# Optimization experiments

Measured on AMD Instinct MI355X. Metric: run time of the kernel, lower is better.

The kernel has to match this reference:

```python
import jax, jax.numpy as jnp
import numpy as np

B = 1024          # batch
H = 512           # hidden_dim
T = 256           # seq_len
CD = 2            # coord_dim
LAT = 64 + 64 + 128  # total latent dim


def setup_inputs() -> dict:
    key = jax.random.key(0)
    ks = jax.random.split(key, 20)
    s = 0.05  # weight init scale
    rn = lambda k, shp: (jax.random.normal(k, shp, dtype=jnp.float32) * s)
    return {
        "z_primitive": jax.random.normal(ks[0], (B, 64), dtype=jnp.float32),
        "z_skill": jax.random.normal(ks[1], (B, 64), dtype=jnp.float32),
        "z_style": jax.random.normal(ks[2], (B, 128), dtype=jnp.float32),
        "W_proj": rn(ks[3], (2 * H, LAT)),
        "b_proj": jnp.zeros((2 * H,), jnp.float32),
        "Wih1": rn(ks[4], (4 * H, CD)),
        "Whh1": rn(ks[5], (4 * H, H)),
        "bih1": jnp.zeros((4 * H,), jnp.float32),
        "bhh1": jnp.zeros((4 * H,), jnp.float32),
        "Wih2": rn(ks[6], (4 * H, H)),
        "Whh2": rn(ks[7], (4 * H, H)),
        "bih2": jnp.zeros((4 * H,), jnp.float32),
        "bhh2": jnp.zeros((4 * H,), jnp.float32),
        "Wo1": rn(ks[8], (H // 2, H)),
        "bo1": jnp.zeros((H // 2,), jnp.float32),
        "Wo2": rn(ks[9], (CD, H // 2)),
        "bo2": jnp.zeros((CD,), jnp.float32),
    }


def _lstm_cell(x, h, c, Wih, Whh, bih, bhh):
    # PyTorch gate order: i, f, g, o
    gates = x @ Wih.T + h @ Whh.T + (bih + bhh)
    i, f, g, o = jnp.split(gates, 4, axis=1)
    c_new = jax.nn.sigmoid(f) * c + jax.nn.sigmoid(i) * jnp.tanh(g)
    h_new = jax.nn.sigmoid(o) * jnp.tanh(c_new)
    return h_new, c_new


def reference(z_primitive, z_skill, z_style, W_proj, b_proj,
              Wih1, Whh1, bih1, bhh1, Wih2, Whh2, bih2, bhh2,
              Wo1, bo1, Wo2, bo2):
    z = jnp.concatenate([z_primitive, z_skill, z_style], axis=1)  # [B, LAT]
    init = z @ W_proj.T + b_proj                                  # [B, 2H]
    h0 = init[:, :H]
    c0 = init[:, H:]
    x0 = jnp.zeros((z.shape[0], CD), init.dtype)

    def step(carry, _):
        x, h1, c1, h2, c2 = carry
        h1, c1 = _lstm_cell(x, h1, c1, Wih1, Whh1, bih1, bhh1)
        h2, c2 = _lstm_cell(h1, h2, c2, Wih2, Whh2, bih2, bhh2)
        # output MLP (Dropout inactive in eval)
        y = jax.nn.relu(h2 @ Wo1.T + bo1) @ Wo2.T + bo2  # [B, CD]
        return (y, h1, c1, h2, c2), y

    # h0/c0 repeated across both LSTM layers (repeat(2,1,1) in torch)
    _, ys = jax.lax.scan(step, (x0, h0, c0, h0, c0), None, length=T)
    return jnp.transpose(ys, (1, 0, 2))  # [B, T, CD]
```

## Files before the change

kernel.cpp:

```cpp
#include <hip/hip_runtime.h>
#include <math.h>

#define NB 1024
#define NH 512
#define NT 256
#define NCD 2

typedef unsigned short u16;
typedef __bf16 bf16x8 __attribute__((ext_vector_type(8)));
typedef float  f32x4  __attribute__((ext_vector_type(4)));

#define MFMA_BF16 __builtin_amdgcn_mfma_f32_16x16x32_bf16

__device__ __forceinline__ float sigf(float x) { return 1.0f / (1.0f + expf(-x)); }
__device__ __forceinline__ u16 f2b(float f) {
    union { float f; unsigned i; } v; v.f = f;
    unsigned r = v.i + 0x7fffu + ((v.i >> 16) & 1u);
    return (u16)(r >> 16);
}

__device__ __forceinline__ void async_cp16(const void* gptr, void* lptr) {
    __builtin_amdgcn_global_load_lds(
        (const __attribute__((address_space(1))) unsigned int*)gptr,
        (__attribute__((address_space(3))) unsigned int*)lptr,
        16, 0, 0);
}

__device__ __forceinline__ float aloadf(const float* p) {
    return __hip_atomic_load((float*)p, __ATOMIC_RELAXED, __HIP_MEMORY_SCOPE_AGENT);
}

__global__ __launch_bounds__(256) void convert3(
    const float* __restrict__ a, const float* __restrict__ b,
    const float* __restrict__ c,
    u16* __restrict__ oa, u16* __restrict__ ob, u16* __restrict__ oc)
{
    const int i = blockIdx.x * 256 + threadIdx.x;
    oa[i] = f2b(a[i]); ob[i] = f2b(b[i]); oc[i] = f2b(c[i]);
}

__global__ __launch_bounds__(256) void convw1(
    const float* __restrict__ a, u16* __restrict__ o)
{
    const int i = blockIdx.x * 256 + threadIdx.x;
    o[i] = f2b(a[i]);
}

__global__ __launch_bounds__(256) void bsum_k(
    const float* __restrict__ bi1, const float* __restrict__ bh1,
    const float* __restrict__ bi2, const float* __restrict__ bh2,
    float* __restrict__ o1, float* __restrict__ o2)
{
    const int i = blockIdx.x * 256 + threadIdx.x;
    o1[i] = bi1[i] + bh1[i];
    o2[i] = bi2[i] + bh2[i];
}

__global__ __launch_bounds__(512) void zero_bar(unsigned* __restrict__ b)
{
    b[threadIdx.x] = 0u;
}

__global__ __launch_bounds__(512) void zero_out(float* __restrict__ o)
{
    o[blockIdx.x * 512 + threadIdx.x] = 0.f;
}

__global__ __launch_bounds__(256) void init_kernel(
    const float* __restrict__ zp, const float* __restrict__ zs,
    const float* __restrict__ zst, const float* __restrict__ Wp,
    const float* __restrict__ bp,
    u16* __restrict__ h1, float* __restrict__ c1,
    u16* __restrict__ h2, float* __restrict__ c2)
{
    __shared__ float z[4][256];
    const int tid = threadIdx.x;
    const int b0  = blockIdx.x * 4;
    for (int i = tid; i < 4 * 256; i += 256) {
        const int bb = i >> 8, k = i & 255;
        float v;
        if (k < 64)       v = zp [(b0 + bb) * 64  + k];
        else if (k < 128) v = zs [(b0 + bb) * 64  + (k - 64)];
        else              v = zst[(b0 + bb) * 128 + (k - 128)];
        z[bb][k] = v;
    }
    __syncthreads();
    for (int rt = 0; rt < 4; ++rt) {
        const int r = rt * 256 + tid;
        const float bias = bp[r];
        float a0 = bias, a1 = bias, a2 = bias, a3 = bias;
        for (int k = 0; k < 256; ++k) {
            const float w = Wp[r * 256 + k];
            a0 += z[0][k] * w; a1 += z[1][k] * w;
            a2 += z[2][k] * w; a3 += z[3][k] * w;
        }
        const float acc[4] = {a0, a1, a2, a3};
        for (int bb = 0; bb < 4; ++bb) {
            const int b = b0 + bb;
            if (r < NH) {
                h1[b * NH + r] = f2b(acc[bb]);
                h2[b * NH + r] = f2b(acc[bb]);
            } else {
                c1[b * NH + r - NH] = acc[bb];
                c2[b * NH + r - NH] = acc[bb];
            }
        }
    }
}

__global__ __launch_bounds__(512, 4) void fused_out_lstm1(
    const u16* __restrict__ h2prev,
    const u16* __restrict__ A0,
    const u16* __restrict__ W0,
    const float* __restrict__ bsum,
    const float* __restrict__ Wx,
    const u16* __restrict__ W1b,
    const float* __restrict__ bo1, const float* __restrict__ Wo2,
    const float* __restrict__ bo2, float* __restrict__ outp,
    float* __restrict__ c, u16* __restrict__ hnext,
    unsigned* __restrict__ bar,
    const int t, const int do_lstm)
{
    __shared__ __align__(16) char smem[61440];
    float* eg  = (float*)smem;

    const int tid  = threadIdx.x;
    const int lane = tid & 63;
    const int wv   = tid >> 6;
    const int g    = wv & 3;
    const int mh   = wv >> 2;
    const int l15  = lane & 15;
    const int q    = lane >> 4;
    const int bx   = blockIdx.x;
    const int ut   = (bx & 7) * 2 + ((bx >> 3) & 1);
    const int grp  = bx >> 4;
    const int b0   = grp * 32;
    const int u0   = ut * 32;

    int goffW0, goffW1, goffA = 0, goffWS = 0;
    {
        const int c0 = (wv * 2) * 64 + lane;
        const int w0r = c0 >> 3;
        goffW0 = ((w0r >> 5) * NH + u0 + (w0r & 31)) * NH + (((c0 & 7) ^ (w0r & 7)) * 8);
        const int c1i = (wv * 2 + 1) * 64 + lane;
        const int w1r = c1i >> 3;
        goffW1 = ((w1r >> 5) * NH + u0 + (w1r & 31)) * NH + (((c1i & 7) ^ (w1r & 7)) * 8);
        if (wv < 4) {
            const int ca = wv * 64 + lane;
            const int ar = ca >> 3;
            goffA = (b0 + ar) * NH + (((ca & 7) ^ (ar & 7)) * 8);
        }
        if (wv == 4 || wv == 5) {
            const int cs = (wv - 4) * 64 + lane;
            const int rl = cs >> 3;
            goffWS = (ut * 16 + rl) * NH + (((cs & 7) ^ (rl & 7)) * 8);
        }
    }

    auto issue = [&](int m, int bi) {
        const int k0 = (m & 7) * 64;
        char* base = smem + bi * 20480;
        async_cp16((const void*)(W0 + goffW0 + k0),
                   (void*)(base + 4096 + (wv * 2) * 1024));
        async_cp16((const void*)(W0 + goffW1 + k0),
                   (void*)(base + 4096 + (wv * 2 + 1) * 1024));
        if (wv < 4)
            async_cp16((const void*)(A0 + goffA + k0),
                       (void*)(base + wv * 1024));
    };

    const int u_e  = tid & 31;
    const int bq_e = tid >> 5;
    const int ug_e = u0 + u_e;
    float bs[4], wx0[4], wx1[4], cpre[2];
#pragma unroll
    for (int g4 = 0; g4 < 4; ++g4) bs[g4] = bsum[g4 * NH + ug_e];
#pragma unroll
    for (int g4 = 0; g4 < 4; ++g4) {
        wx0[g4] = Wx[(g4 * NH + ug_e) * 2 + 0];
        wx1[g4] = Wx[(g4 * NH + ug_e) * 2 + 1];
    }
    cpre[0] = c[(size_t)(b0 + bq_e * 2 + 0) * NH + ug_e];
    cpre[1] = c[(size_t)(b0 + bq_e * 2 + 1) * NH + ug_e];

    if (do_lstm) issue(0, 2);

    if (h2prev) {
        f32x4 acc_o[2];
        acc_o[0] = (f32x4){0.f, 0.f, 0.f, 0.f};
        acc_o[1] = (f32x4){0.f, 0.f, 0.f, 0.f};

        auto issue_pa = [&](int k, int pb) {
            const int k0 = k * 64;
            char* base = smem + pb * 8192;
            if (wv < 4)
                async_cp16((const void*)(h2prev + goffA + k0),
                           (void*)(base + (wv << 10)));
            if (wv == 4 || wv == 5)
                async_cp16((const void*)(W1b + goffWS + k0),
                           (void*)(base + 4096 + ((wv - 4) << 10)));
        };
        issue_pa(0, 0);
        issue_pa(1, 1);
        int cp = 0;
        for (int kk = 0; kk < 8; ++kk) {
            if (kk + 1 < 8)
                asm volatile("s_waitcnt vmcnt(1)" ::: "memory");
            else
                asm volatile("s_waitcnt vmcnt(0)" ::: "memory");
            __builtin_amdgcn_s_barrier();
            if (kk + 2 < 8) {
                int pb = cp + 2; if (pb >= 3) pb -= 3;
                issue_pa(kk + 2, pb);
            }
            const char* pbase = smem + cp * 8192;
#pragma unroll
            for (int kh = 0; kh < 2; ++kh) {
                const int j = (kh * 4 + q) ^ (l15 & 7);
                const bf16x8 bfr = *(const bf16x8*)(pbase + 4096 + l15 * 128 + j * 16);
#pragma unroll
                for (int mi = 0; mi < 2; ++mi) {
                    const bf16x8 av = *(const bf16x8*)(pbase + (mi * 16 + l15) * 128 + j * 16);
                    acc_o[mi] = MFMA_BF16(av, bfr, acc_o[mi], 0, 0, 0);
                }
            }
            ++cp; if (cp == 3) cp = 0;
        }
        const int ng = ut * 16 + l15;
        const float bo1n = bo1[ng];
        const float w20  = Wo2[ng];
        const float w21  = Wo2[256 + ng];
        float pa[2][4], pb[2][4];
#pragma unroll
        for (int mi = 0; mi < 2; ++mi)
#pragma unroll
            for (int r = 0; r < 4; ++r) {
                const float s = fmaxf(acc_o[mi][r] + bo1n, 0.f);
                pa[mi][r] = s * w20;
                pb[mi][r] = s * w21;
            }
#pragma unroll
        for (int off = 1; off < 16; off <<= 1)
#pragma unroll
            for (int mi = 0; mi < 2; ++mi)
#pragma unroll
                for (int r = 0; r < 4; ++r) {
                    pa[mi][r] += __shfl_xor(pa[mi][r], off, 64);
                    pb[mi][r] += __shfl_xor(pb[mi][r], off, 64);
                }
        if (wv == 0 && l15 == 0) {
            const float b20 = (ut == 0) ? bo2[0] : 0.f;
            const float b21 = (ut == 0) ? bo2[1] : 0.f;
#pragma unroll
            for (int mi = 0; mi < 2; ++mi)
#pragma unroll
                for (int r = 0; r < 4; ++r) {
                    const int m = mi * 16 + q * 4 + r;
                    float* dst = outp + (size_t)(b0 + m) * (NT * NCD) + (t - 1) * NCD;
                    atomicAdd(dst + 0, pa[mi][r] + b20);
                    atomicAdd(dst + 1, pb[mi][r] + b21);
                }
        }
        __syncthreads();
    }
    if (!do_lstm) return;

    f32x4 acc[2];
    acc[0] = (f32x4){0.f, 0.f, 0.f, 0.f};
    acc[1] = (f32x4){0.f, 0.f, 0.f, 0.f};
    const int M = 8;
    issue(1, 0);
    int ci = 2;
    for (int m = 0; m < M; ++m) {
        if (m + 1 < M) {
            if (wv < 4) asm volatile("s_waitcnt vmcnt(3)" ::: "memory");
            else        asm volatile("s_waitcnt vmcnt(2)" ::: "memory");
        } else {
            asm volatile("s_waitcnt vmcnt(0)" ::: "memory");
        }
        __builtin_amdgcn_s_barrier();
        if (m + 2 < M) {
            int bi = ci + 2; if (bi >= 3) bi -= 3;
            issue(m + 2, bi);
        }
        const char* bA = smem + ci * 20480;
        const char* bW = bA + 4096;
#pragma unroll
        for (int khi = 0; khi < 2; ++khi) {
            bf16x8 bfr[2];
#pragma unroll
            for (int ni = 0; ni < 2; ++ni) {
                const int wrow = g * 32 + ni * 16 + l15;
                const int j = (khi * 4 + q) ^ (wrow & 7);
                bfr[ni] = *(const bf16x8*)(bW + wrow * 128 + j * 16);
            }
            const int row = mh * 16 + l15;
            const int j = (khi * 4 + q) ^ (row & 7);
            const bf16x8 av = *(const bf16x8*)(bA + row * 128 + j * 16);
            acc[0] = MFMA_BF16(av, bfr[0], acc[0], 0, 0, 0);
            acc[1] = MFMA_BF16(av, bfr[1], acc[1], 0, 0, 0);
        }
        ++ci; if (ci == 3) ci = 0;
    }

    float r_x[4] = {0.f, 0.f, 0.f, 0.f};
    if (h2prev) {
        unsigned* mybar = bar + grp * 16;
        const unsigned target = 16u * (unsigned)t;
        __syncthreads();
        if (tid == 0) {
            __hip_atomic_fetch_add(mybar, 1u, __ATOMIC_RELAXED, __HIP_MEMORY_SCOPE_AGENT);
            int guard = 0;
            while (__hip_atomic_load(mybar, __ATOMIC_RELAXED, __HIP_MEMORY_SCOPE_AGENT)
                       < target && ++guard < (1 << 20)) {
                __builtin_amdgcn_s_sleep(1);
            }
        }
        __syncthreads();
#pragma unroll
        for (int jj = 0; jj < 2; ++jj) {
            const float* src = outp + (size_t)(b0 + bq_e * 2 + jj) * (NT * NCD)
                               + (t - 1) * NCD;
            r_x[jj * 2 + 0] = aloadf(src + 0);
            r_x[jj * 2 + 1] = aloadf(src + 1);
        }
    }

    __syncthreads();
#pragma unroll
    for (int ni = 0; ni < 2; ++ni)
#pragma unroll
        for (int r = 0; r < 4; ++r)
            eg[(g * 32 + mh * 16 + q * 4 + r) * 33 + ni * 16 + l15] = acc[ni][r];
    __syncthreads();

#pragma unroll
    for (int jj = 0; jj < 2; ++jj) {
        const int bl = bq_e * 2 + jj;
        const int b  = b0 + bl;
        float gv[4];
#pragma unroll
        for (int g4 = 0; g4 < 4; ++g4) gv[g4] = eg[(g4 * 32 + bl) * 33 + u_e] + bs[g4];
        const float x0 = r_x[jj * 2 + 0];
        const float x1 = r_x[jj * 2 + 1];
#pragma unroll
        for (int g4 = 0; g4 < 4; ++g4) gv[g4] += x0 * wx0[g4] + x1 * wx1[g4];
        const float iv = sigf(gv[0]);
        const float fv = sigf(gv[1]);
        const float gg = tanhf(gv[2]);
        const float ov = sigf(gv[3]);
        const size_t idx = (size_t)b * NH + ug_e;
        const float cn = fv * cpre[jj] + iv * gg;
        c[idx] = cn;
        hnext[idx] = f2b(ov * tanhf(cn));
    }
}

__global__ __launch_bounds__(512, 4) void lstm_mfma32(
    const u16* __restrict__ A0, const u16* __restrict__ W0,
    const u16* __restrict__ A1, const u16* __restrict__ W1,
    const float* __restrict__ bsum,
    float* __restrict__ c, u16* __restrict__ hnext,
    const int npass)
{
    __shared__ __align__(16) char smem[61440];
    float* eg = (float*)smem;

    const int tid  = threadIdx.x;
    const int lane = tid & 63;
    const int wv   = tid >> 6;
    const int g    = wv & 3;
    const int mh   = wv >> 2;
    const int l15  = lane & 15;
    const int q    = lane >> 4;
    const int bx   = blockIdx.x;
    const int ut   = (bx & 7) * 2 + ((bx >> 3) & 1);
    const int grp  = bx >> 4;
    const int b0   = grp * 32;
    const int u0   = ut * 32;

    int goffW0, goffW1, goffA = 0;
    {
        const int c0 = (wv * 2) * 64 + lane;
        const int w0r = c0 >> 3;
        goffW0 = ((w0r >> 5) * NH + u0 + (w0r & 31)) * NH + (((c0 & 7) ^ (w0r & 7)) * 8);
        const int c1i = (wv * 2 + 1) * 64 + lane;
        const int w1r = c1i >> 3;
        goffW1 = ((w1r >> 5) * NH + u0 + (w1r & 31)) * NH + (((c1i & 7) ^ (w1r & 7)) * 8);
        if (wv < 4) {
            const int ca = wv * 64 + lane;
            const int ar = ca >> 3;
            goffA = (b0 + ar) * NH + (((ca & 7) ^ (ar & 7)) * 8);
        }
    }

    const int u_e  = tid & 31;
    const int bq_e = tid >> 5;
    const int ug_e = u0 + u_e;
    float bs[4], cpre[2];
#pragma unroll
    for (int g4 = 0; g4 < 4; ++g4) bs[g4] = bsum[g4 * NH + ug_e];
    cpre[0] = c[(size_t)(b0 + bq_e * 2 + 0) * NH + ug_e];
    cpre[1] = c[(size_t)(b0 + bq_e * 2 + 1) * NH + ug_e];

    f32x4 acc[2];
    acc[0] = (f32x4){0.f, 0.f, 0.f, 0.f};
    acc[1] = (f32x4){0.f, 0.f, 0.f, 0.f};

    const int M = npass * 8;

    auto issue = [&](int m, int bi) {
        const u16* __restrict__ Ap = (m < 8) ? A0 : A1;
        const u16* __restrict__ Wp = (m < 8) ? W0 : W1;
        const int k0 = (m & 7) * 64;
        char* base = smem + bi * 20480;
        async_cp16((const void*)(Wp + goffW0 + k0),
                   (void*)(base + 4096 + (wv * 2) * 1024));
        async_cp16((const void*)(Wp + goffW1 + k0),
                   (void*)(base + 4096 + (wv * 2 + 1) * 1024));
        if (wv < 4)
            async_cp16((const void*)(Ap + goffA + k0),
                       (void*)(base + wv * 1024));
    };

    issue(0, 0);
    if (M > 1) issue(1, 1);
    int ci = 0;
    for (int m = 0; m < M; ++m) {
        if (m + 1 < M) {
            if (wv < 4) asm volatile("s_waitcnt vmcnt(3)" ::: "memory");
            else        asm volatile("s_waitcnt vmcnt(2)" ::: "memory");
        } else {
            asm volatile("s_waitcnt vmcnt(0)" ::: "memory");
        }
        __builtin_amdgcn_s_barrier();
        if (m + 2 < M) {
            int bi = ci + 2; if (bi >= 3) bi -= 3;
            issue(m + 2, bi);
        }
        const char* bA = smem + ci * 20480;
        const char* bW = bA + 4096;
#pragma unroll
        for (int khi = 0; khi < 2; ++khi) {
            bf16x8 bfr[2];
#pragma unroll
            for (int ni = 0; ni < 2; ++ni) {
                const int wrow = g * 32 + ni * 16 + l15;
                const int j = (khi * 4 + q) ^ (wrow & 7);
                bfr[ni] = *(const bf16x8*)(bW + wrow * 128 + j * 16);
            }
            const int row = mh * 16 + l15;
            const int j = (khi * 4 + q) ^ (row & 7);
            const bf16x8 av = *(const bf16x8*)(bA + row * 128 + j * 16);
            acc[0] = MFMA_BF16(av, bfr[0], acc[0], 0, 0, 0);
            acc[1] = MFMA_BF16(av, bfr[1], acc[1], 0, 0, 0);
        }
        ++ci; if (ci == 3) ci = 0;
    }

    __syncthreads();
#pragma unroll
    for (int ni = 0; ni < 2; ++ni)
#pragma unroll
        for (int r = 0; r < 4; ++r)
            eg[(g * 32 + mh * 16 + q * 4 + r) * 33 + ni * 16 + l15] = acc[ni][r];
    __syncthreads();

#pragma unroll
    for (int jj = 0; jj < 2; ++jj) {
        const int bl = bq_e * 2 + jj;
        const int b  = b0 + bl;
        float gv[4];
#pragma unroll
        for (int g4 = 0; g4 < 4; ++g4) gv[g4] = eg[(g4 * 32 + bl) * 33 + u_e] + bs[g4];
        const float iv = sigf(gv[0]);
        const float fv = sigf(gv[1]);
        const float gg = tanhf(gv[2]);
        const float ov = sigf(gv[3]);
        const size_t idx = (size_t)b * NH + ug_e;
        const float cn = fv * cpre[jj] + iv * gg;
        c[idx] = cn;
        hnext[idx] = f2b(ov * tanhf(cn));
    }
}

extern "C" void kernel_launch(void* const* d_in, const int* in_sizes, int n_in,
                              void* d_out, int out_size, void* d_ws, size_t ws_size,
                              hipStream_t stream)
{
    const float* zp   = (const float*)d_in[0];
    const float* zsk  = (const float*)d_in[1];
    const float* zst  = (const float*)d_in[2];
    const float* Wp   = (const float*)d_in[3];
    const float* bp   = (const float*)d_in[4];
    const float* Wih1 = (const float*)d_in[5];
    const float* Whh1 = (const float*)d_in[6];
    const float* bih1 = (const float*)d_in[7];
    const float* bhh1 = (const float*)d_in[8];
    const float* Wih2 = (const float*)d_in[9];
    const float* Whh2 = (const float*)d_in[10];
    const float* bih2 = (const float*)d_in[11];
    const float* bhh2 = (const float*)d_in[12];
    const float* Wo1  = (const float*)d_in[13];
    const float* bo1  = (const float*)d_in[14];
    const float* Wo2  = (const float*)d_in[15];
    const float* bo2  = (const float*)d_in[16];

    const size_t BH = (size_t)NB * NH;
    u16*   h1a   = (u16*)d_ws;
    u16*   h1b   = h1a + BH;
    u16*   h2a   = h1b + BH;
    u16*   h2b   = h2a + BH;
    float* c1    = (float*)(h2b + BH);
    float* c2    = c1 + BH;
    float* bs1   = c2 + BH;
    float* bs2   = bs1 + 2048;
    u16*   Wo1b  = (u16*)(bs2 + 2048);
    u16*   Whh1b = Wo1b + 131072;
    u16*   Wih2b = Whh1b + 1048576;
    u16*   Whh2b = Wih2b + 1048576;
    unsigned* bar = (unsigned*)(Whh2b + 1048576);

    convert3<<<(2048 * 512) / 256, 256, 0, stream>>>(Whh1, Wih2, Whh2, Whh1b, Wih2b, Whh2b);
    convw1<<<(256 * 512) / 256, 256, 0, stream>>>(Wo1, Wo1b);
    bsum_k<<<2048 / 256, 256, 0, stream>>>(bih1, bhh1, bih2, bhh2, bs1, bs2);
    init_kernel<<<NB / 4, 256, 0, stream>>>(zp, zsk, zst, Wp, bp, h1a, c1, h2a, c2);
    zero_bar<<<1, 512, 0, stream>>>(bar);
    zero_out<<<(NB * NT * NCD) / 512, 512, 0, stream>>>((float*)d_out);

    u16* h1c = h1a; u16* h1n = h1b;
    u16* h2c = h2a; u16* h2n = h2b;
    float* outp = (float*)d_out;
    for (int t = 0; t < NT; ++t) {
        fused_out_lstm1<<<512, 512, 0, stream>>>(
            (t == 0) ? (const u16*)0 : h2c, h1c, Whh1b, bs1, Wih1,
            Wo1b, bo1, Wo2, bo2, outp, c1, h1n, bar, t, 1);
        lstm_mfma32<<<512, 512, 0, stream>>>(h1n, Wih2b, h2c, Whh2b,
                                             bs2, c2, h2n, 2);
        u16* tmp = h1c; h1c = h1n; h1n = tmp;
        tmp = h2c; h2c = h2n; h2n = tmp;
    }
    fused_out_lstm1<<<512, 512, 0, stream>>>(
        h2c, h1c, Whh1b, bs1, Wih1,
        Wo1b, bo1, Wo2, bo2, outp, c1, h1n, bar, NT, 0);
}
```

Measured before the change: 7.121 ms.

## Fuse output-MLP GEMM and LSTM gate GEMM into one interleaved K loop

Merges the previous step's output projection (h2prev × Wo1) and the current LSTM recurrent GEMM into a single 8-iteration K loop that shares one barrier per iteration. The LSTM stream moves to double buffering in separate smem regions, so the two async-copy streams prefetch together instead of running as serial phases. The gate-store to LDS is also moved ahead of the cross-block barrier wait so it overlaps the spin. The cost is a more fragile vmcnt accounting: the mixed waits fall back to vmcnt(0) in many cases, and LSTM prefetch depth drops from two stages to one.

```diff
diff --git a/kernel.cpp b/kernel.cpp
--- a/kernel.cpp
+++ b/kernel.cpp
@@ -136,6 +136,7 @@
     const int grp  = bx >> 4;
     const int b0   = grp * 32;
     const int u0   = ut * 32;
+    const bool has_prev = (h2prev != 0);
 
     int goffW0, goffW1, goffA = 0, goffWS = 0;
     {
@@ -157,9 +158,9 @@
         }
     }
 
-    auto issue = [&](int m, int bi) {
+    auto issueL = [&](int m, int s) {
         const int k0 = (m & 7) * 64;
-        char* base = smem + bi * 20480;
+        char* base = smem + s * 20480;
         async_cp16((const void*)(W0 + goffW0 + k0),
                    (void*)(base + 4096 + (wv * 2) * 1024));
         async_cp16((const void*)(W0 + goffW1 + k0),
@@ -168,6 +169,16 @@
             async_cp16((const void*)(A0 + goffA + k0),
                        (void*)(base + wv * 1024));
     };
+    auto issue_pa = [&](int k, int pb) {
+        const int k0 = k * 64;
+        char* base = smem + 40960 + pb * 6144;
+        if (wv < 4)
+            async_cp16((const void*)(h2prev + goffA + k0),
+                       (void*)(base + (wv << 10)));
+        if (wv == 4 || wv == 5)
+            async_cp16((const void*)(W1b + goffWS + k0),
+                       (void*)(base + 4096 + ((wv - 4) << 10)));
+    };
 
     const int u_e  = tid & 31;
     const int bq_e = tid >> 5;
@@ -183,37 +194,29 @@
     cpre[0] = c[(size_t)(b0 + bq_e * 2 + 0) * NH + ug_e];
     cpre[1] = c[(size_t)(b0 + bq_e * 2 + 1) * NH + ug_e];
 
-    if (do_lstm) issue(0, 2);
-
-    if (h2prev) {
-        f32x4 acc_o[2];
-        acc_o[0] = (f32x4){0.f, 0.f, 0.f, 0.f};
-        acc_o[1] = (f32x4){0.f, 0.f, 0.f, 0.f};
-
-        auto issue_pa = [&](int k, int pb) {
-            const int k0 = k * 64;
-            char* base = smem + pb * 8192;
-            if (wv < 4)
-                async_cp16((const void*)(h2prev + goffA + k0),
-                           (void*)(base + (wv << 10)));
-            if (wv == 4 || wv == 5)
-                async_cp16((const void*)(W1b + goffWS + k0),
-                           (void*)(base + 4096 + ((wv - 4) << 10)));
-        };
-        issue_pa(0, 0);
-        issue_pa(1, 1);
-        int cp = 0;
-        for (int kk = 0; kk < 8; ++kk) {
-            if (kk + 1 < 8)
-                asm volatile("s_waitcnt vmcnt(1)" ::: "memory");
-            else
-                asm volatile("s_waitcnt vmcnt(0)" ::: "memory");
-            __builtin_amdgcn_s_barrier();
-            if (kk + 2 < 8) {
-                int pb = cp + 2; if (pb >= 3) pb -= 3;
-                issue_pa(kk + 2, pb);
-            }
-            const char* pbase = smem + cp * 8192;
+    f32x4 acc_o[2], acc[2];
+    acc_o[0] = (f32x4){0.f, 0.f, 0.f, 0.f};
+    acc_o[1] = (f32x4){0.f, 0.f, 0.f, 0.f};
+    acc[0]   = (f32x4){0.f, 0.f, 0.f, 0.f};
+    acc[1]   = (f32x4){0.f, 0.f, 0.f, 0.f};
+
+    if (do_lstm) issueL(0, 0);
+    if (has_prev) { issue_pa(0, 0); issue_pa(1, 1); }
+
+    for (int k = 0; k < 8; ++k) {
+        if (has_prev && k < 7 && wv < 6)
+            asm volatile("s_waitcnt vmcnt(1)" ::: "memory");
+        else
+            asm volatile("s_waitcnt vmcnt(0)" ::: "memory");
+        __builtin_amdgcn_s_barrier();
+        if (do_lstm && k + 1 < 8) issueL(k + 1, (k + 1) & 1);
+        if (has_prev && k + 2 < 8) {
+            int pb = k + 2; while (pb >= 3) pb -= 3;
+            issue_pa(k + 2, pb);
+        }
+        if (has_prev) {
+            int cp = k; while (cp >= 3) cp -= 3;
+            const char* pbase = smem + 40960 + cp * 6144;
 #pragma unroll
             for (int kh = 0; kh < 2; ++kh) {
                 const int j = (kh * 4 + q) ^ (l15 & 7);
@@ -224,8 +227,29 @@
                     acc_o[mi] = MFMA_BF16(av, bfr, acc_o[mi], 0, 0, 0);
                 }
             }
-            ++cp; if (cp == 3) cp = 0;
-        }
+        }
+        if (do_lstm) {
+            const char* bA = smem + (k & 1) * 20480;
+            const char* bW = bA + 4096;
+#pragma unroll
+            for (int khi = 0; khi < 2; ++khi) {
+                bf16x8 bfr[2];
+#pragma unroll
+                for (int ni = 0; ni < 2; ++ni) {
+                    const int wrow = g * 32 + ni * 16 + l15;
+                    const int j = (khi * 4 + q) ^ (wrow & 7);
+                    bfr[ni] = *(const bf16x8*)(bW + wrow * 128 + j * 16);
+                }
+                const int row = mh * 16 + l15;
+                const int j = (khi * 4 + q) ^ (row & 7);
+                const bf16x8 av = *(const bf16x8*)(bA + row * 128 + j * 16);
+                acc[0] = MFMA_BF16(av, bfr[0], acc[0], 0, 0, 0);
+                acc[1] = MFMA_BF16(av, bfr[1], acc[1], 0, 0, 0);
+            }
+        }
+    }
+
+    if (has_prev) {
         const int ng = ut * 16 + l15;
         const float bo1n = bo1[ng];
         const float w20  = Wo2[ng];
@@ -261,53 +285,21 @@
                     atomicAdd(dst + 1, pb[mi][r] + b21);
                 }
         }
-        __syncthreads();
     }
     if (!do_lstm) return;
 
-    f32x4 acc[2];
-    acc[0] = (f32x4){0.f, 0.f, 0.f, 0.f};
-    acc[1] = (f32x4){0.f, 0.f, 0.f, 0.f};
-    const int M = 8;
-    issue(1, 0);
-    int ci = 2;
-    for (int m = 0; m < M; ++m) {
-        if (m + 1 < M) {
-            if (wv < 4) asm volatile("s_waitcnt vmcnt(3)" ::: "memory");
-            else        asm volatile("s_waitcnt vmcnt(2)" ::: "memory");
-        } else {
-            asm volatile("s_waitcnt vmcnt(0)" ::: "memory");
-        }
-        __builtin_amdgcn_s_barrier();
-        if (m + 2 < M) {
-            int bi = ci + 2; if (bi >= 3) bi -= 3;
-            issue(m + 2, bi);
-        }
-        const char* bA = smem + ci * 20480;
-        const char* bW = bA + 4096;
-#pragma unroll
-        for (int khi = 0; khi < 2; ++khi) {
-            bf16x8 bfr[2];
-#pragma unroll
-            for (int ni = 0; ni < 2; ++ni) {
-                const int wrow = g * 32 + ni * 16 + l15;
-                const int j = (khi * 4 + q) ^ (wrow & 7);
-                bfr[ni] = *(const bf16x8*)(bW + wrow * 128 + j * 16);
-            }
-            const int row = mh * 16 + l15;
-            const int j = (khi * 4 + q) ^ (row & 7);
-            const bf16x8 av = *(const bf16x8*)(bA + row * 128 + j * 16);
-            acc[0] = MFMA_BF16(av, bfr[0], acc[0], 0, 0, 0);
-            acc[1] = MFMA_BF16(av, bfr[1], acc[1], 0, 0, 0);
-        }
-        ++ci; if (ci == 3) ci = 0;
-    }
+    __syncthreads();
+#pragma unroll
+    for (int ni = 0; ni < 2; ++ni)
+#pragma unroll
+        for (int r = 0; r < 4; ++r)
+            eg[(g * 32 + mh * 16 + q * 4 + r) * 33 + ni * 16 + l15] = acc[ni][r];
+    __syncthreads();
 
     float r_x[4] = {0.f, 0.f, 0.f, 0.f};
-    if (h2prev) {
+    if (has_prev) {
         unsigned* mybar = bar + grp * 16;
         const unsigned target = 16u * (unsigned)t;
-        __syncthreads();
         if (tid == 0) {
             __hip_atomic_fetch_add(mybar, 1u, __ATOMIC_RELAXED, __HIP_MEMORY_SCOPE_AGENT);
             int guard = 0;
@@ -325,14 +317,6 @@
             r_x[jj * 2 + 1] = aloadf(src + 1);
         }
     }
-
-    __syncthreads();
-#pragma unroll
-    for (int ni = 0; ni < 2; ++ni)
-#pragma unroll
-        for (int r = 0; r < 4; ++r)
-            eg[(g * 32 + mh * 16 + q * 4 + r) * 33 + ni * 16 + l15] = acc[ni][r];
-    __syncthreads();
 
 #pragma unroll
     for (int jj = 0; jj < 2; ++jj) {
```

Result: faster. 6.824 ms (-4.2%).
